# Kernel optimization log

Measured on AMD Instinct MI355X. Metric: run time of the kernel, lower is better.

## Reference

```python
import jax, jax.numpy as jnp
import numpy as np
from jax import lax

HEADS = 8
LN_EPS = 1e-5


def setup_inputs() -> dict:
    key = jax.random.key(0)
    k = jax.random.split(key, 8)
    B, C, H, W, r = 4, 64, 64, 64, 4
    T = H * W
    x = jax.random.normal(k[0], (B, C, H, W), dtype=jnp.float32)
    conv_w = jax.random.normal(k[1], (C, C, r, r), dtype=jnp.float32) * 0.02  # OIHW
    conv_b = jnp.zeros((C,), dtype=jnp.float32)
    ln_g = jnp.ones((C,), dtype=jnp.float32)
    ln_b = jnp.zeros((C,), dtype=jnp.float32)
    Wqkv = jax.random.normal(k[2], (C, 3 * C), dtype=jnp.float32) * 0.02  # to_qvk (no bias)
    W0 = jax.random.normal(k[3], (C, C), dtype=jnp.float32) * 0.02  # output proj (no bias)
    E = jax.random.normal(k[4], (T, T // 4), dtype=jnp.float32)  # Linformer proj (randn in torch fwd)
    return {"x": x, "conv_w": conv_w, "conv_b": conv_b, "ln_g": ln_g,
            "ln_b": ln_b, "Wqkv": Wqkv, "W0": W0, "E": E}


def _layernorm2d(y, g, b):
    # LayerNorm over channel dim of NCHW (torch: permute to NHWC, LN last dim)
    yt = y.transpose(0, 2, 3, 1)  # b h w c
    mu = yt.mean(-1, keepdims=True)
    var = ((yt - mu) ** 2).mean(-1, keepdims=True)
    yt = (yt - mu) * lax.rsqrt(var + LN_EPS) * g + b
    return yt.transpose(0, 3, 1, 2)


def reference(x, conv_w, conv_b, ln_g, ln_b, Wqkv, W0, E):
    B, C, H, W = x.shape
    T = H * W
    dh = C // HEADS
    r = conv_w.shape[-1]

    # reducer: conv(stride=r) + LayerNorm2d. NOTE: faithful to the torch module,
    # this result is computed but NEVER used by the output (dead code in source).
    red = lax.conv_general_dilated(x, conv_w, (r, r), 'VALID',
                                   dimension_numbers=('NCHW', 'OIHW', 'NCHW'))
    red = red + conv_b[None, :, None, None]
    _red = _layernorm2d(red, ln_g, ln_b)  # unused, matches source

    # tokens from full-resolution x: b c h w -> b (h w) c
    xf = x.reshape(B, C, T).transpose(0, 2, 1)  # [B,T,C]
    qkv = xf @ Wqkv  # [B,T,3C]
    # rearrange 'b t (d k h)' with k=3, h=HEADS -> composite order (d, k, h)
    qkv = qkv.reshape(B, T, dh, 3, HEADS)
    q = qkv[:, :, :, 0, :].transpose(0, 3, 1, 2)  # [B,h,T,d]
    kk = qkv[:, :, :, 1, :].transpose(0, 3, 1, 2)
    v = qkv[:, :, :, 2, :].transpose(0, 3, 1, 2)

    # Linformer low-rank projection of V and K: [B,h,T,d] x [T,k] -> [B,h,k,d]
    v = jnp.einsum('bhjd,jk->bhkd', v, E)
    kk = jnp.einsum('bhjd,jk->bhkd', kk, E)

    scale = dh ** -0.5
    scores = jnp.einsum('bhid,bhjd->bhij', q, kk) * scale  # [B,h,T,k]
    attn = jax.nn.softmax(scores, axis=-1)
    out = jnp.einsum('bhij,bhjd->bhid', attn, v)  # [B,h,T,d]

    out = out.transpose(0, 2, 1, 3).reshape(B, T, C)  # b h i d -> b i (h d)
    out = out @ W0  # [B,T,C]
    return out.transpose(0, 2, 1).reshape(B, C, H, W)
```

## Files before the change

### kernel.cpp

```cpp
#include <hip/hip_runtime.h>

#define T_DIM 4096
#define KD    1024
#define SCALE 0.35355339059327373f

typedef __attribute__((ext_vector_type(8))) short bf16x8;
typedef __attribute__((ext_vector_type(4))) short bf16x4;
typedef __attribute__((ext_vector_type(4))) float f32x4;

__device__ inline unsigned short f2bf(float f) {
  unsigned u = __float_as_uint(f);
  unsigned r = u + 0x7fffu + ((u >> 16) & 1u);
  return (unsigned short)(r >> 16);
}

__device__ inline unsigned cvt_pk_bf16(float a, float b) {
  unsigned ua = __float_as_uint(a); ua += 0x7fffu + ((ua >> 16) & 1u);
  unsigned ub = __float_as_uint(b); ub += 0x7fffu + ((ub >> 16) & 1u);
  return (ua >> 16) | (ub & 0xffff0000u);
}

__device__ inline unsigned pk_trunc(float a, float b) {
  return (__float_as_uint(a) >> 16) | (__float_as_uint(b) & 0xffff0000u);
}

__device__ inline bf16x4 mk4(unsigned lo, unsigned hi) {
  union { unsigned u[2]; bf16x4 v; } x; x.u[0] = lo; x.u[1] = hi; return x.v;
}

__device__ inline bf16x8 mk8(unsigned a, unsigned b, unsigned c, unsigned d) {
  union { unsigned u[4]; bf16x8 v; } x;
  x.u[0] = a; x.u[1] = b; x.u[2] = c; x.u[3] = d; return x.v;
}

__device__ inline f32x4 mfma16(bf16x4 a, bf16x4 b, f32x4 c) {
  bf16x8 a8 = {}, b8 = {};
  a8[0] = a[0]; a8[1] = a[1]; a8[2] = a[2]; a8[3] = a[3];
  b8[0] = b[0]; b8[1] = b[1]; b8[2] = b[2]; b8[3] = b[3];
  return __builtin_amdgcn_mfma_f32_16x16x32_bf16(a8, b8, c, 0, 0, 0);
}

__global__ __launch_bounds__(256) void k_front(const float* __restrict__ x,
                                               const float* __restrict__ E,
                                               const float* __restrict__ Wqkv,
                                               float* __restrict__ partial,
                                               float* __restrict__ Q) {
  const int bid = blockIdx.x;
  const int tid = threadIdx.x;

  if (bid < 512) {
    const int kb = bid & 7;
    const int b  = (bid >> 3) & 3;
    const int s  = bid >> 5;
    const int k0 = kb * 128;
    const int lane = tid & 63;
    const int w = tid >> 6;
    const int li = lane & 15, lg = lane >> 4;

    f32x4 acc[4][2] = {};
#pragma unroll 2
    for (int tb = 0; tb < 8; ++tb) {
      const int tbase = s * 256 + tb * 32 + lg * 8;
      bf16x8 bq[2];
#pragma unroll
      for (int nt = 0; nt < 2; ++nt) {
        const int kcol = k0 + w * 32 + nt * 16 + li;
        float bv[8];
#pragma unroll
        for (int j = 0; j < 8; ++j)
          bv[j] = E[(size_t)(tbase + j) * KD + kcol];
        bq[nt] = mk8(cvt_pk_bf16(bv[0], bv[1]), cvt_pk_bf16(bv[2], bv[3]),
                     cvt_pk_bf16(bv[4], bv[5]), cvt_pk_bf16(bv[6], bv[7]));
      }
#pragma unroll
      for (int mt = 0; mt < 4; ++mt) {
        const float* ap = x + ((size_t)b * 64 + mt * 16 + li) * T_DIM + tbase;
        float4 a0 = *(const float4*)(ap);
        float4 a1 = *(const float4*)(ap + 4);
        bf16x8 af8 = mk8(cvt_pk_bf16(a0.x, a0.y), cvt_pk_bf16(a0.z, a0.w),
                         cvt_pk_bf16(a1.x, a1.y), cvt_pk_bf16(a1.z, a1.w));
        acc[mt][0] = __builtin_amdgcn_mfma_f32_16x16x32_bf16(af8, bq[0], acc[mt][0], 0, 0, 0);
        acc[mt][1] = __builtin_amdgcn_mfma_f32_16x16x32_bf16(af8, bq[1], acc[mt][1], 0, 0, 0);
      }
    }
    float* pb = partial + ((size_t)s * 4 + b) * (64 * KD);
#pragma unroll
    for (int mt = 0; mt < 4; ++mt)
#pragma unroll
      for (int nt = 0; nt < 2; ++nt) {
        const int row = mt * 16 + lg * 4;
        const int col = k0 + w * 32 + nt * 16 + li;
#pragma unroll
        for (int reg = 0; reg < 4; ++reg)
          pb[(size_t)(row + reg) * KD + col] = acc[mt][nt][reg];
      }
  } else {
    const int idx = bid - 512;
    const int g  = idx & 7;
    const int tt = (idx >> 3) & 15;
    const int b  = idx >> 7;
    const int t  = tt * 256 + tid;
    const int col0 = g * 24;

    float acc[8];
#pragma unroll
    for (int j = 0; j < 8; ++j) acc[j] = 0.f;
    const float* xb = x + (size_t)b * 64 * T_DIM + t;
#pragma unroll 4
    for (int c = 0; c < 64; ++c) {
      float xv = xb[(size_t)c * T_DIM];
      const float* wr = Wqkv + c * 192 + col0;
#pragma unroll
      for (int h = 0; h < 8; ++h) acc[h] += xv * wr[h];
    }
#pragma unroll
    for (int h = 0; h < 8; ++h)
      Q[(((size_t)(b * 8 + h)) * 8 + g) * T_DIM + t] = acc[h];
  }
}

__global__ __launch_bounds__(256) void k_xered(const float* __restrict__ partial,
                                               unsigned short* __restrict__ XP) {
  const size_t o = ((size_t)blockIdx.x * 256 + threadIdx.x) * 4;
  float4 a = make_float4(0.f, 0.f, 0.f, 0.f);
#pragma unroll
  for (int s = 0; s < 16; ++s) {
    float4 v = *(const float4*)(partial + ((size_t)s * 4) * (64 * KD) + o);
    a.x += v.x; a.y += v.y; a.z += v.z; a.w += v.w;
  }
  *(uint2*)(XP + o) = make_uint2(cvt_pk_bf16(a.x, a.y), cvt_pk_bf16(a.z, a.w));
}

__global__ __launch_bounds__(256) void k_kvp(const unsigned short* __restrict__ XP,
                                             const float* __restrict__ Wqkv,
                                             uint2* __restrict__ Kg,
                                             unsigned short* __restrict__ Vg) {
  const int kb  = blockIdx.x;
  const int h   = blockIdx.y;
  const int b   = blockIdx.z;
  const int sel = threadIdx.x >> 7;
  const int k   = kb * 128 + (threadIdx.x & 127);

  float acc[8];
#pragma unroll
  for (int d = 0; d < 8; ++d) acc[d] = 0.f;
  const unsigned short* xb = XP + (size_t)b * 64 * KD + k;
#pragma unroll 4
  for (int c = 0; c < 64; ++c) {
    float xv = __uint_as_float((unsigned)xb[(size_t)c * KD] << 16);
    const float* wr = Wqkv + c * 192 + (sel + 1) * 8 + h;
#pragma unroll
    for (int d = 0; d < 8; ++d) acc[d] += xv * wr[d * 24];
  }
  const int bh = b * 8 + h;
  if (sel == 0) {
    uint2* kg = Kg + (size_t)bh * 2048;
    kg[k] = make_uint2(cvt_pk_bf16(acc[0] * SCALE, acc[1] * SCALE),
                       cvt_pk_bf16(acc[2] * SCALE, acc[3] * SCALE));
    kg[1024 + k] = make_uint2(cvt_pk_bf16(acc[4] * SCALE, acc[5] * SCALE),
                              cvt_pk_bf16(acc[6] * SCALE, acc[7] * SCALE));
  } else {
#pragma unroll
    for (int d = 0; d < 8; ++d)
      Vg[(size_t)(bh * 8 + d) * KD + k] = f2bf(acc[d]);
  }
}

#define VT_PITCH 1032
__global__ __launch_bounds__(256) void k_attn(const float* __restrict__ Q,
                                              const uint2* __restrict__ Kg,
                                              const unsigned short* __restrict__ Vg,
                                              float* __restrict__ O) {
  __shared__ unsigned short Kt[2 * 1024 * 4];
  __shared__ unsigned short Vt[9 * VT_PITCH];
  const int bh = blockIdx.x;
  const int tid = threadIdx.x;

  const uint2* kg = Kg + (size_t)bh * 2048;
  uint2* kt2 = (uint2*)Kt;
#pragma unroll
  for (int it = 0; it < 8; ++it)
    kt2[it * 256 + tid] = kg[it * 256 + tid];
  const unsigned* vg = (const unsigned*)(Vg + (size_t)bh * 8192);
#pragma unroll
  for (int dd = 0; dd < 8; ++dd) {
#pragma unroll
    for (int it = 0; it < 2; ++it) {
      const int j2 = it * 256 + tid;
      *(unsigned*)(Vt + dd * VT_PITCH + j2 * 2) = vg[dd * 512 + j2];
    }
  }
#pragma unroll
  for (int it = 0; it < 2; ++it)
    *(unsigned*)(Vt + 8 * VT_PITCH + (it * 256 + tid) * 2) = 0x3F803F80u;
  __syncthreads();

  const int lane = tid & 63, w = tid >> 6;
  const int li = lane & 15, lg = lane >> 4;
  const int i0w = blockIdx.y * 128 + w * 32;

  bf16x4 qf[2] = {bf16x4{}, bf16x4{}};
  if (lane < 32) {
#pragma unroll
    for (int it2 = 0; it2 < 2; ++it2) {
      const float* qp = Q + ((size_t)bh * 8 + lg * 4) * T_DIM + i0w + it2 * 16 + li;
      qf[it2] = mk4(cvt_pk_bf16(qp[0], qp[T_DIM]),
                    cvt_pk_bf16(qp[2 * T_DIM], qp[3 * T_DIM]));
    }
  }

  f32x4 accO[2] = {f32x4{0.f, 0.f, 0.f, 0.f}, f32x4{0.f, 0.f, 0.f, 0.f}};
#pragma unroll 2
  for (int jt = 0; jt < 1024; jt += 16) {
    bf16x4 kf = {};
    if (lane < 32) kf = *(const bf16x4*)(&Kt[(size_t)(lg * 1024 + jt + li) * 4]);
    bf16x4 vf = {};
    if (li < 9) vf = *(const bf16x4*)(&Vt[li * VT_PITCH + jt + lg * 4]);
#pragma unroll
    for (int it2 = 0; it2 < 2; ++it2) {
      f32x4 st = mfma16(kf, qf[it2], f32x4{0.f, 0.f, 0.f, 0.f});
      f32x4 p;
      p[0] = __expf(st[0]); p[1] = __expf(st[1]);
      p[2] = __expf(st[2]); p[3] = __expf(st[3]);
      bf16x4 pf = mk4(pk_trunc(p[0], p[1]), pk_trunc(p[2], p[3]));
      accO[it2] = mfma16(vf, pf, accO[it2]);
    }
  }

  const int b = bh >> 3, h = bh & 7;
#pragma unroll
  for (int it2 = 0; it2 < 2; ++it2) {
    float l = __shfl(accO[it2][0], 32 + li);
    float inv = 1.0f / l;
    if (lane < 32) {
      const int i = i0w + it2 * 16 + li;
      float4 o = make_float4(accO[it2][0] * inv, accO[it2][1] * inv,
                             accO[it2][2] * inv, accO[it2][3] * inv);
      *(float4*)(O + ((size_t)b * T_DIM + i) * 64 + h * 8 + lg * 4) = o;
    }
  }
}

__global__ __launch_bounds__(256) void k_out(const float* __restrict__ O,
                                             const float* __restrict__ W0,
                                             float* __restrict__ out) {
  const int cg_ = blockIdx.x;
  const int tt = blockIdx.y;
  const int b  = blockIdx.z;
  const int t  = tt * 256 + threadIdx.x;
  const int col0 = cg_ * 8;

  float acc[8];
#pragma unroll
  for (int j = 0; j < 8; ++j) acc[j] = 0.f;
  const float* orow = O + ((size_t)b * T_DIM + t) * 64;
#pragma unroll
  for (int c0 = 0; c0 < 64; c0 += 4) {
    float4 v = *(const float4*)(orow + c0);
    float ov[4] = {v.x, v.y, v.z, v.w};
#pragma unroll
    for (int u = 0; u < 4; ++u) {
      const float* wr = W0 + (c0 + u) * 64 + col0;
#pragma unroll
      for (int j = 0; j < 8; ++j) acc[j] += ov[u] * wr[j];
    }
  }
#pragma unroll
  for (int j = 0; j < 8; ++j)
    out[((size_t)b * 64 + col0 + j) * T_DIM + t] = acc[j];
}

extern "C" void kernel_launch(void* const* d_in, const int* in_sizes, int n_in,
                              void* d_out, int out_size, void* d_ws, size_t ws_size,
                              hipStream_t stream) {
  const float* x    = (const float*)d_in[0];
  const float* Wqkv = (const float*)d_in[5];
  const float* W0   = (const float*)d_in[6];
  const float* E    = (const float*)d_in[7];
  float* out = (float*)d_out;

  float* Q           = (float*)d_ws;
  float* O           = Q + 1048576;
  float* partial     = O + 1048576;
  unsigned short* XP = (unsigned short*)(partial + 4194304);
  uint2* Kg          = (uint2*)(XP + 262144);
  unsigned short* Vg = (unsigned short*)(Kg + 65536);

  k_front <<<dim3(1024),     256, 0, stream>>>(x, E, Wqkv, partial, Q);
  k_xered <<<dim3(256),      256, 0, stream>>>(partial, XP);
  k_kvp   <<<dim3(8, 8, 4),  256, 0, stream>>>(XP, Wqkv, Kg, Vg);
  k_attn  <<<dim3(32, 32),   256, 0, stream>>>(Q, Kg, Vg, O);
  k_out   <<<dim3(8, 16, 4), 256, 0, stream>>>(O, W0, out);
}
```

Measured before the change: 154.0 us.

## Fuse partial reduction into K/V projection and attention with output projection

Merges the split-K partial reduction into the K/V projection kernel, staging the reduced bf16 X tile in shared memory. Attention is restructured so each block handles one batch and 64 query rows across all 8 heads. The head outputs are kept in shared memory as bf16 and the W0 projection is applied with an MFMA, removing the O round-trip through global memory and two launches. The costs are that K/V tiles are reloaded per head inside each block, the partial sums are now re-read by every head block (8x redundant reads), and the attention grid drops to 256 blocks.

Measured after the change: 180.7 us. 1.17x slower.

```diff
diff --git a/kernel.cpp b/kernel.cpp
--- a/kernel.cpp
+++ b/kernel.cpp
@@ -119,155 +119,154 @@
   }
 }
 
-__global__ __launch_bounds__(256) void k_xered(const float* __restrict__ partial,
-                                               unsigned short* __restrict__ XP) {
-  const size_t o = ((size_t)blockIdx.x * 256 + threadIdx.x) * 4;
-  float4 a = make_float4(0.f, 0.f, 0.f, 0.f);
-#pragma unroll
-  for (int s = 0; s < 16; ++s) {
-    float4 v = *(const float4*)(partial + ((size_t)s * 4) * (64 * KD) + o);
-    a.x += v.x; a.y += v.y; a.z += v.z; a.w += v.w;
-  }
-  *(uint2*)(XP + o) = make_uint2(cvt_pk_bf16(a.x, a.y), cvt_pk_bf16(a.z, a.w));
-}
-
-__global__ __launch_bounds__(256) void k_kvp(const unsigned short* __restrict__ XP,
+__global__ __launch_bounds__(256) void k_xkv(const float* __restrict__ partial,
                                              const float* __restrict__ Wqkv,
                                              uint2* __restrict__ Kg,
                                              unsigned short* __restrict__ Vg) {
-  const int kb  = blockIdx.x;
-  const int h   = blockIdx.y;
-  const int b   = blockIdx.z;
-  const int sel = threadIdx.x >> 7;
-  const int k   = kb * 128 + (threadIdx.x & 127);
-
-  float acc[8];
-#pragma unroll
-  for (int d = 0; d < 8; ++d) acc[d] = 0.f;
-  const unsigned short* xb = XP + (size_t)b * 64 * KD + k;
+  __shared__ unsigned short XPs[64 * 72];
+  const int kb = blockIdx.x;
+  const int h  = blockIdx.y;
+  const int b  = blockIdx.z;
+  const int tid = threadIdx.x;
+
+  {
+    const int kk = tid & 63;
+    const int cg = tid >> 6;
+#pragma unroll
+    for (int u = 0; u < 16; ++u) {
+      const int c = cg * 16 + u;
+      const size_t src = (size_t)c * KD + kb * 64 + kk;
+      float a = 0.f;
+#pragma unroll
+      for (int s = 0; s < 16; ++s)
+        a += partial[((size_t)s * 4 + b) * (64 * KD) + src];
+      XPs[c * 72 + kk] = f2bf(a);
+    }
+  }
+  __syncthreads();
+
+  const int klocal = tid & 63;
+  const int sel    = (tid >> 6) & 1;
+  const int dg     = tid >> 7;
+  const int k      = kb * 64 + klocal;
+
+  float acc[4];
+#pragma unroll
+  for (int d = 0; d < 4; ++d) acc[d] = 0.f;
 #pragma unroll 4
   for (int c = 0; c < 64; ++c) {
-    float xv = __uint_as_float((unsigned)xb[(size_t)c * KD] << 16);
+    float xv = __uint_as_float((unsigned)XPs[c * 72 + klocal] << 16);
     const float* wr = Wqkv + c * 192 + (sel + 1) * 8 + h;
 #pragma unroll
-    for (int d = 0; d < 8; ++d) acc[d] += xv * wr[d * 24];
-  }
+    for (int d = 0; d < 4; ++d) acc[d] += xv * wr[(dg * 4 + d) * 24];
+  }
+
   const int bh = b * 8 + h;
   if (sel == 0) {
     uint2* kg = Kg + (size_t)bh * 2048;
-    kg[k] = make_uint2(cvt_pk_bf16(acc[0] * SCALE, acc[1] * SCALE),
-                       cvt_pk_bf16(acc[2] * SCALE, acc[3] * SCALE));
-    kg[1024 + k] = make_uint2(cvt_pk_bf16(acc[4] * SCALE, acc[5] * SCALE),
-                              cvt_pk_bf16(acc[6] * SCALE, acc[7] * SCALE));
+    kg[dg * 1024 + k] = make_uint2(cvt_pk_bf16(acc[0] * SCALE, acc[1] * SCALE),
+                                   cvt_pk_bf16(acc[2] * SCALE, acc[3] * SCALE));
   } else {
 #pragma unroll
-    for (int d = 0; d < 8; ++d)
-      Vg[(size_t)(bh * 8 + d) * KD + k] = f2bf(acc[d]);
+    for (int d = 0; d < 4; ++d)
+      Vg[(size_t)(bh * 8 + dg * 4 + d) * KD + k] = f2bf(acc[d]);
   }
 }
 
 #define VT_PITCH 1032
-__global__ __launch_bounds__(256) void k_attn(const float* __restrict__ Q,
-                                              const uint2* __restrict__ Kg,
-                                              const unsigned short* __restrict__ Vg,
-                                              float* __restrict__ O) {
+#define OT_PITCH 72
+__global__ __launch_bounds__(256) void k_ao(const float* __restrict__ Q,
+                                            const uint2* __restrict__ Kg,
+                                            const unsigned short* __restrict__ Vg,
+                                            const float* __restrict__ W0,
+                                            float* __restrict__ out) {
   __shared__ unsigned short Kt[2 * 1024 * 4];
   __shared__ unsigned short Vt[9 * VT_PITCH];
-  const int bh = blockIdx.x;
+  __shared__ unsigned short Ot[4 * 16 * OT_PITCH];
+  const int bid = blockIdx.x;
+  const int b  = bid >> 6;
+  const int iy = bid & 63;
   const int tid = threadIdx.x;
-
-  const uint2* kg = Kg + (size_t)bh * 2048;
-  uint2* kt2 = (uint2*)Kt;
-#pragma unroll
-  for (int it = 0; it < 8; ++it)
-    kt2[it * 256 + tid] = kg[it * 256 + tid];
-  const unsigned* vg = (const unsigned*)(Vg + (size_t)bh * 8192);
-#pragma unroll
-  for (int dd = 0; dd < 8; ++dd) {
-#pragma unroll
-    for (int it = 0; it < 2; ++it) {
-      const int j2 = it * 256 + tid;
-      *(unsigned*)(Vt + dd * VT_PITCH + j2 * 2) = vg[dd * 512 + j2];
-    }
-  }
-#pragma unroll
-  for (int it = 0; it < 2; ++it)
-    *(unsigned*)(Vt + 8 * VT_PITCH + (it * 256 + tid) * 2) = 0x3F803F80u;
-  __syncthreads();
-
   const int lane = tid & 63, w = tid >> 6;
   const int li = lane & 15, lg = lane >> 4;
-  const int i0w = blockIdx.y * 128 + w * 32;
-
-  bf16x4 qf[2] = {bf16x4{}, bf16x4{}};
-  if (lane < 32) {
-#pragma unroll
-    for (int it2 = 0; it2 < 2; ++it2) {
-      const float* qp = Q + ((size_t)bh * 8 + lg * 4) * T_DIM + i0w + it2 * 16 + li;
-      qf[it2] = mk4(cvt_pk_bf16(qp[0], qp[T_DIM]),
-                    cvt_pk_bf16(qp[2 * T_DIM], qp[3 * T_DIM]));
-    }
-  }
-
-  f32x4 accO[2] = {f32x4{0.f, 0.f, 0.f, 0.f}, f32x4{0.f, 0.f, 0.f, 0.f}};
+  const int i0w = iy * 64 + w * 16;
+  unsigned short* OtW = Ot + w * 16 * OT_PITCH;
+
+  for (int h = 0; h < 8; ++h) {
+    const int bh = b * 8 + h;
+    __syncthreads();
+    const uint2* kg = Kg + (size_t)bh * 2048;
+    uint2* kt2 = (uint2*)Kt;
+#pragma unroll
+    for (int it = 0; it < 8; ++it)
+      kt2[it * 256 + tid] = kg[it * 256 + tid];
+    const unsigned* vg = (const unsigned*)(Vg + (size_t)bh * 8192);
+#pragma unroll
+    for (int dd = 0; dd < 8; ++dd) {
+#pragma unroll
+      for (int it = 0; it < 2; ++it) {
+        const int j2 = it * 256 + tid;
+        *(unsigned*)(Vt + dd * VT_PITCH + j2 * 2) = vg[dd * 512 + j2];
+      }
+    }
+#pragma unroll
+    for (int it = 0; it < 2; ++it)
+      *(unsigned*)(Vt + 8 * VT_PITCH + (it * 256 + tid) * 2) = 0x3F803F80u;
+    __syncthreads();
+
+    bf16x4 qf = {};
+    if (lane < 32) {
+      const float* qp = Q + ((size_t)bh * 8 + lg * 4) * T_DIM + i0w + li;
+      qf = mk4(cvt_pk_bf16(qp[0], qp[T_DIM]),
+               cvt_pk_bf16(qp[2 * T_DIM], qp[3 * T_DIM]));
+    }
+
+    f32x4 accO = {0.f, 0.f, 0.f, 0.f};
 #pragma unroll 2
-  for (int jt = 0; jt < 1024; jt += 16) {
-    bf16x4 kf = {};
-    if (lane < 32) kf = *(const bf16x4*)(&Kt[(size_t)(lg * 1024 + jt + li) * 4]);
-    bf16x4 vf = {};
-    if (li < 9) vf = *(const bf16x4*)(&Vt[li * VT_PITCH + jt + lg * 4]);
-#pragma unroll
-    for (int it2 = 0; it2 < 2; ++it2) {
-      f32x4 st = mfma16(kf, qf[it2], f32x4{0.f, 0.f, 0.f, 0.f});
+    for (int jt = 0; jt < 1024; jt += 16) {
+      bf16x4 kf = {};
+      if (lane < 32) kf = *(const bf16x4*)(&Kt[(size_t)(lg * 1024 + jt + li) * 4]);
+      bf16x4 vf = {};
+      if (li < 9) vf = *(const bf16x4*)(&Vt[li * VT_PITCH + jt + lg * 4]);
+      f32x4 st = mfma16(kf, qf, f32x4{0.f, 0.f, 0.f, 0.f});
       f32x4 p;
       p[0] = __expf(st[0]); p[1] = __expf(st[1]);
       p[2] = __expf(st[2]); p[3] = __expf(st[3]);
       bf16x4 pf = mk4(pk_trunc(p[0], p[1]), pk_trunc(p[2], p[3]));
-      accO[it2] = mfma16(vf, pf, accO[it2]);
-    }
-  }
-
-  const int b = bh >> 3, h = bh & 7;
-#pragma unroll
-  for (int it2 = 0; it2 < 2; ++it2) {
-    float l = __shfl(accO[it2][0], 32 + li);
+      accO = mfma16(vf, pf, accO);
+    }
+
+    float l = __shfl(accO[0], 32 + li);
     float inv = 1.0f / l;
     if (lane < 32) {
-      const int i = i0w + it2 * 16 + li;
-      float4 o = make_float4(accO[it2][0] * inv, accO[it2][1] * inv,
-                             accO[it2][2] * inv, accO[it2][3] * inv);
-      *(float4*)(O + ((size_t)b * T_DIM + i) * 64 + h * 8 + lg * 4) = o;
-    }
-  }
-}
-
-__global__ __launch_bounds__(256) void k_out(const float* __restrict__ O,
-                                             const float* __restrict__ W0,
-                                             float* __restrict__ out) {
-  const int cg_ = blockIdx.x;
-  const int tt = blockIdx.y;
-  const int b  = blockIdx.z;
-  const int t  = tt * 256 + threadIdx.x;
-  const int col0 = cg_ * 8;
-
-  float acc[8];
-#pragma unroll
-  for (int j = 0; j < 8; ++j) acc[j] = 0.f;
-  const float* orow = O + ((size_t)b * T_DIM + t) * 64;
-#pragma unroll
-  for (int c0 = 0; c0 < 64; c0 += 4) {
-    float4 v = *(const float4*)(orow + c0);
-    float ov[4] = {v.x, v.y, v.z, v.w};
-#pragma unroll
-    for (int u = 0; u < 4; ++u) {
-      const float* wr = W0 + (c0 + u) * 64 + col0;
-#pragma unroll
-      for (int j = 0; j < 8; ++j) acc[j] += ov[u] * wr[j];
-    }
-  }
-#pragma unroll
-  for (int j = 0; j < 8; ++j)
-    out[((size_t)b * 64 + col0 + j) * T_DIM + t] = acc[j];
+      unsigned p0 = cvt_pk_bf16(accO[0] * inv, accO[1] * inv);
+      unsigned p1 = cvt_pk_bf16(accO[2] * inv, accO[3] * inv);
+      *(uint2*)(OtW + li * OT_PITCH + h * 8 + lg * 4) = make_uint2(p0, p1);
+    }
+  }
+
+  f32x4 ao[4] = {};
+#pragma unroll
+  for (int ks = 0; ks < 2; ++ks) {
+    bf16x8 bo = *(const bf16x8*)(OtW + li * OT_PITCH + ks * 32 + lg * 8);
+#pragma unroll
+    for (int mt = 0; mt < 4; ++mt) {
+      float wv[8];
+#pragma unroll
+      for (int j = 0; j < 8; ++j)
+        wv[j] = W0[(size_t)(ks * 32 + lg * 8 + j) * 64 + mt * 16 + li];
+      bf16x8 aw = mk8(cvt_pk_bf16(wv[0], wv[1]), cvt_pk_bf16(wv[2], wv[3]),
+                      cvt_pk_bf16(wv[4], wv[5]), cvt_pk_bf16(wv[6], wv[7]));
+      ao[mt] = __builtin_amdgcn_mfma_f32_16x16x32_bf16(aw, bo, ao[mt], 0, 0, 0);
+    }
+  }
+#pragma unroll
+  for (int mt = 0; mt < 4; ++mt) {
+    const int c = mt * 16 + lg * 4;
+#pragma unroll
+    for (int reg = 0; reg < 4; ++reg)
+      out[((size_t)b * 64 + c + reg) * T_DIM + i0w + li] = ao[mt][reg];
+  }
 }
 
 extern "C" void kernel_launch(void* const* d_in, const int* in_sizes, int n_in,
@@ -280,15 +279,11 @@
   float* out = (float*)d_out;
 
   float* Q           = (float*)d_ws;
-  float* O           = Q + 1048576;
-  float* partial     = O + 1048576;
-  unsigned short* XP = (unsigned short*)(partial + 4194304);
-  uint2* Kg          = (uint2*)(XP + 262144);
+  float* partial     = Q + 1048576;
+  uint2* Kg          = (uint2*)(partial + 4194304);
   unsigned short* Vg = (unsigned short*)(Kg + 65536);
 
   k_front <<<dim3(1024),     256, 0, stream>>>(x, E, Wqkv, partial, Q);
-  k_xered <<<dim3(256),      256, 0, stream>>>(partial, XP);
-  k_kvp   <<<dim3(8, 8, 4),  256, 0, stream>>>(XP, Wqkv, Kg, Vg);
-  k_attn  <<<dim3(32, 32),   256, 0, stream>>>(Q, Kg, Vg, O);
-  k_out   <<<dim3(8, 16, 4), 256, 0, stream>>>(O, W0, out);
-}
+  k_xkv   <<<dim3(16, 8, 4), 256, 0, stream>>>(partial, Wqkv, Kg, Vg);
+  k_ao    <<<dim3(256),      256, 0, stream>>>(Q, Kg, Vg, W0, out);
+}
```
